# Kernel optimization log

Hardware: AMD Instinct MI355X
Metric: run time of the kernel (lower is better)

Reference implementation:

```python
import jax, jax.numpy as jnp
import numpy as np

EMBED_DIM = 1024
HEADS = 16
D_HEAD = EMBED_DIM // HEADS
B, S = 4, 2048


def setup_inputs() -> dict:
    key = jax.random.key(0)
    ks = jax.random.split(key, 7)
    scale = 1.0 / np.sqrt(EMBED_DIM)
    inp = {
        "key": jax.random.normal(ks[0], (B, S, EMBED_DIM), jnp.float32),
        "query": jax.random.normal(ks[1], (B, S, EMBED_DIM), jnp.float32),
        "value": jax.random.normal(ks[2], (B, S, EMBED_DIM), jnp.float32),
        # causal boolean mask, broadcastable to [B, H, S, S]
        "mask": jnp.tril(jnp.ones((S, S), dtype=bool))[None, None, :, :] * jnp.ones((B, 1, 1, 1), dtype=bool),
        # nn.Linear weights, stored torch-style as [out_features, in_features]
        "Wq": jax.random.normal(ks[3], (EMBED_DIM, EMBED_DIM), jnp.float32) * scale,
        "Wk": jax.random.normal(ks[4], (EMBED_DIM, EMBED_DIM), jnp.float32) * scale,
        "Wv": jax.random.normal(ks[5], (EMBED_DIM, EMBED_DIM), jnp.float32) * scale,
        "Wo": jax.random.normal(ks[6], (EMBED_DIM, EMBED_DIM), jnp.float32) * scale,
    }
    return inp


def reference(key, query, value, mask, Wq, Wk, Wv, Wo):
    # projections (nn.Linear, bias=False): x @ W.T
    q = query @ Wq.T                                    # [B,S,E]
    k = key @ Wk.T
    v = value @ Wv.T
    # split heads -> [B,H,S,d]
    def split(x):
        return x.reshape(B, S, HEADS, D_HEAD).transpose(0, 2, 1, 3)
    q, k, v = split(q), split(k), split(v)
    # scaled dot-product scores [B,H,S,S]
    scores = jnp.einsum("bhqd,bhkd->bhqk", q, k) / np.sqrt(D_HEAD).astype(np.float32)
    scores = jnp.where(mask, scores, jnp.float32(-1e9))
    attn = jax.nn.softmax(scores, axis=-1)
    # attention output, merge heads
    out = jnp.einsum("bhqk,bhkd->bhqd", attn, v)        # [B,H,S,d]
    out = out.transpose(0, 2, 1, 3).reshape(B, S, EMBED_DIM)
    return out @ Wo.T
```

## Files before the change

kernel.cpp:

```cpp
#include <hip/hip_runtime.h>

#define SEQ 2048
#define EMBED 1024
#define DHEAD 64

typedef _Float16 h8 __attribute__((ext_vector_type(8)));
typedef _Float16 h4 __attribute__((ext_vector_type(4)));
typedef float f4 __attribute__((ext_vector_type(4)));
typedef unsigned int u32;

__device__ __forceinline__ void gload_lds16(const void* g, void* l) {
    __builtin_amdgcn_global_load_lds(
        (const __attribute__((address_space(1))) u32*)g,
        (__attribute__((address_space(3))) u32*)l, 16, 0, 0);
}

__global__ __launch_bounds__(256) void cvt_f16(
    const float* __restrict__ q, const float* __restrict__ k, const float* __restrict__ v,
    const float* __restrict__ wq, const float* __restrict__ wk, const float* __restrict__ wv,
    const float* __restrict__ wo,
    _Float16* __restrict__ q16, _Float16* __restrict__ k16, _Float16* __restrict__ v16,
    _Float16* __restrict__ wq16, _Float16* __restrict__ wk16, _Float16* __restrict__ wv16,
    _Float16* __restrict__ wo16)
{
    int bid = blockIdx.x;
    const float* src;
    _Float16* dst;
    float scale = 1.0f;
    size_t base;
    if (bid < 24576) {
        int seg = bid >> 13;
        base = (size_t)(bid & 8191) * 1024 + threadIdx.x * 4;
        src = seg == 0 ? q : seg == 1 ? k : v;
        dst = seg == 0 ? q16 : seg == 1 ? k16 : v16;
    } else {
        int wb = bid - 24576;
        int seg = wb >> 10;
        base = (size_t)(wb & 1023) * 1024 + threadIdx.x * 4;
        src = seg == 0 ? wq : seg == 1 ? wk : seg == 2 ? wv : wo;
        dst = seg == 0 ? wq16 : seg == 1 ? wk16 : seg == 2 ? wv16 : wo16;
        if (seg == 0) scale = 0.18033688011112042f;
    }
    float4 x = *(const float4*)(src + base);
    h4 y = { (_Float16)(x.x * scale), (_Float16)(x.y * scale),
             (_Float16)(x.z * scale), (_Float16)(x.w * scale) };
    *(h4*)(dst + base) = y;
}

__device__ __forceinline__ void gemm_core(const _Float16* __restrict__ A, const _Float16* __restrict__ W,
                                          int m0, int n0, int tid,
                                          _Float16* As, _Float16* Bs, f4 acc[4][4])
{
    const int lane = tid & 63, wave = tid >> 6;
    const int t16 = lane & 15, quad = lane >> 4;
    const int wm = (wave >> 1) * 64, wn = (wave & 1) * 64;
    const int wb = wave * 64;
    const int u0 = tid, u1 = tid + 256;
    const int r0 = u0 >> 2, c0 = u0 & 3;
    const int r1 = u1 >> 2, c1 = u1 & 3;
    const _Float16* ga0 = A + (size_t)(m0 + r0) * 1024 + c0 * 8;
    const _Float16* ga1 = A + (size_t)(m0 + r1) * 1024 + c1 * 8;
    const _Float16* gb0 = W + (size_t)(n0 + r0) * 1024 + c0 * 8;
    const _Float16* gb1 = W + (size_t)(n0 + r1) * 1024 + c1 * 8;
    _Float16* la0 = As + wb * 8;
    _Float16* la1 = As + (256 + wb) * 8;
    _Float16* lb0 = Bs + wb * 8;
    _Float16* lb1 = Bs + (256 + wb) * 8;

    for (int k0 = 0; k0 < 1024; k0 += 32) {
        __syncthreads();
        gload_lds16(ga0 + k0, la0);
        gload_lds16(ga1 + k0, la1);
        gload_lds16(gb0 + k0, lb0);
        gload_lds16(gb1 + k0, lb1);
        __syncthreads();
        h8 af[4], bf[4];
#pragma unroll
        for (int i = 0; i < 4; ++i)
            af[i] = *(const h8*)(As + (wm + i * 16 + t16) * 32 + quad * 8);
#pragma unroll
        for (int j = 0; j < 4; ++j)
            bf[j] = *(const h8*)(Bs + (wn + j * 16 + t16) * 32 + quad * 8);
#pragma unroll
        for (int i = 0; i < 4; ++i)
#pragma unroll
            for (int j = 0; j < 4; ++j)
                acc[i][j] = __builtin_amdgcn_mfma_f32_16x16x32_f16(af[i], bf[j], acc[i][j], 0, 0, 0);
    }
}

__global__ __launch_bounds__(256) void proj_qkv(
    const _Float16* __restrict__ q16, const _Float16* __restrict__ k16, const _Float16* __restrict__ v16,
    const _Float16* __restrict__ Wq, const _Float16* __restrict__ Wk, const _Float16* __restrict__ Wv,
    _Float16* __restrict__ Qh, _Float16* __restrict__ Kh, _Float16* __restrict__ Vt)
{
    __shared__ _Float16 As[4096], Bs[4096];
    const int tid = threadIdx.x;
    const int z = blockIdx.z;
    const _Float16 *A, *W;
    int m0, n0;
    if (z == 2) { A = Wv; W = v16; m0 = blockIdx.y * 128; n0 = blockIdx.x * 128; }
    else if (z == 0) { A = q16; W = Wq; m0 = blockIdx.x * 128; n0 = blockIdx.y * 128; }
    else { A = k16; W = Wk; m0 = blockIdx.x * 128; n0 = blockIdx.y * 128; }

    f4 acc[4][4];
    const f4 z4 = {0.f, 0.f, 0.f, 0.f};
#pragma unroll
    for (int i = 0; i < 4; ++i)
#pragma unroll
        for (int j = 0; j < 4; ++j) acc[i][j] = z4;

    gemm_core(A, W, m0, n0, tid, As, Bs, acc);

    const int lane = tid & 63, wave = tid >> 6;
    const int t16 = lane & 15, quad = lane >> 4;
    const int wm = (wave >> 1) * 64, wn = (wave & 1) * 64;
#pragma unroll
    for (int i = 0; i < 4; ++i)
#pragma unroll
        for (int j = 0; j < 4; ++j)
#pragma unroll
            for (int reg = 0; reg < 4; ++reg) {
                int gm = m0 + wm + i * 16 + quad * 4 + reg;
                int gn = n0 + wn + j * 16 + t16;
                float vv = acc[i][j][reg];
                if (z < 2) {
                    int b = gm >> 11, s = gm & 2047, h = gn >> 6, dd = gn & 63;
                    _Float16* dst = (z == 0) ? Qh : Kh;
                    dst[(((size_t)(b * 16 + h) * SEQ) + s) * DHEAD + dd] = (_Float16)vv;
                } else {
                    int h = gm >> 6, dd = gm & 63, b = gn >> 11, s = gn & 2047;
                    Vt[(((size_t)(b * 16 + h) * DHEAD) + dd) * SEQ + s] = (_Float16)vv;
                }
            }
}

__global__ __launch_bounds__(256) void attn3(
    const _Float16* __restrict__ Qh, const _Float16* __restrict__ Kh,
    const _Float16* __restrict__ Vt, _Float16* __restrict__ Ob)
{
    __shared__ _Float16 Kbuf[2][8][512];
    __shared__ _Float16 Vbuf[2][8][512];
    __shared__ _Float16 Pex[4][2][2][512];

    const int tid = threadIdx.x;
    const int lane = tid & 63, wave = tid >> 6;
    const int t16 = lane & 15, quad = lane >> 4;
    const int bh = blockIdx.x;
    const int b = bh >> 4, h = bh & 15;
    const int qb = (gridDim.y - 1) - blockIdx.y;
    const int q0 = qb * 128;
    const int nqt = qb * 2 + 2;

    const _Float16* Qp = Qh + (size_t)bh * SEQ * DHEAD;
    const _Float16* Kp = Kh + (size_t)bh * SEQ * DHEAD;
    const _Float16* Vp = Vt + (size_t)bh * DHEAD * SEQ;

    const int qlo[2] = { q0 + wave * 32, q0 + wave * 32 + 16 };
    const int last0 = (qlo[0] + 15) >> 6;
    const int last1 = (qlo[1] + 15) >> 6;

    h8 qf[2][2];
#pragma unroll
    for (int qb2 = 0; qb2 < 2; ++qb2)
#pragma unroll
        for (int kc = 0; kc < 2; ++kc)
            qf[qb2][kc] = *(const h8*)(Qp + (size_t)(qlo[qb2] + t16) * 64 + kc * 32 + quad * 8);

    const _Float16* Kl = Kp + t16 * 64 + quad * 8;
    const _Float16* Vl = Vp + t16 * 2048 + quad * 8;

#define STAGE(jt_, bufi)                                                                  \
    do {                                                                                  \
        if (wave < 2) {                                                                   \
            _Pragma("unroll")                                                             \
            for (int i_ = 0; i_ < 4; ++i_) {                                              \
                int g_ = wave * 4 + i_;                                                   \
                gload_lds16(Kl + (jt_) * 4096 + (g_ >> 1) * 1024 + (g_ & 1) * 32,         \
                            &Kbuf[bufi][g_][0]);                                          \
            }                                                                             \
        } else {                                                                          \
            _Pragma("unroll")                                                             \
            for (int i_ = 0; i_ < 4; ++i_) {                                              \
                int g_ = (wave - 2) * 4 + i_;                                             \
                gload_lds16(Vl + (g_ >> 1) * 32768 + (jt_) * 64 + (g_ & 1) * 32,          \
                            &Vbuf[bufi][g_][0]);                                          \
            }                                                                             \
        }                                                                                 \
    } while (0)

    STAGE(0, 0);
    __syncthreads();

    float mv[2] = {-1e30f, -1e30f};
    float lv[2] = {0.f, 0.f};
    f4 o_acc[2][4];
    const f4 z4 = {0.f, 0.f, 0.f, 0.f};
#pragma unroll
    for (int qb2 = 0; qb2 < 2; ++qb2)
#pragma unroll
        for (int dt = 0; dt < 4; ++dt) o_acc[qb2][dt] = z4;

    for (int jt = 0; jt < nqt; ++jt) {
        const int buf = jt & 1;
        if (jt + 1 < nqt) STAGE(jt + 1, buf ^ 1);

        if (jt <= last1) {
            f4 s0[4], s1[4];
#pragma unroll
            for (int j4 = 0; j4 < 4; ++j4) {
                h8 kfa = *(const h8*)(&Kbuf[buf][j4 * 2 + 0][lane * 8]);
                h8 kfb = *(const h8*)(&Kbuf[buf][j4 * 2 + 1][lane * 8]);
                s1[j4] = __builtin_amdgcn_mfma_f32_16x16x32_f16(kfa, qf[1][0], z4, 0, 0, 0);
                s1[j4] = __builtin_amdgcn_mfma_f32_16x16x32_f16(kfb, qf[1][1], s1[j4], 0, 0, 0);
                s0[j4] = __builtin_amdgcn_mfma_f32_16x16x32_f16(kfa, qf[0][0], z4, 0, 0, 0);
                s0[j4] = __builtin_amdgcn_mfma_f32_16x16x32_f16(kfb, qf[0][1], s0[j4], 0, 0, 0);
            }

            auto softmax_store = [&](f4* s, int qb2) {
                const int myq = qlo[qb2] + t16;
                if ((jt << 6) + 63 > myq - t16 + 15 || true) {  }
                if ((jt << 6) + 63 > qlo[qb2]) {
#pragma unroll
                    for (int j4 = 0; j4 < 4; ++j4)
#pragma unroll
                        for (int reg = 0; reg < 4; ++reg) {
                            int kk = (jt << 6) + j4 * 16 + quad * 4 + reg;
                            if (kk > myq) s[j4][reg] = -1e30f;
                        }
                }
                float mr = s[0][0];
#pragma unroll
                for (int j4 = 0; j4 < 4; ++j4)
#pragma unroll
                    for (int reg = 0; reg < 4; ++reg) mr = fmaxf(mr, s[j4][reg]);
                mr = fmaxf(mr, __shfl_xor(mr, 16, 64));
                mr = fmaxf(mr, __shfl_xor(mr, 32, 64));
                float mn = fmaxf(mv[qb2], mr);
                float al = __builtin_amdgcn_exp2f(mv[qb2] - mn);
                mv[qb2] = mn;
                float rs = 0.f;
#pragma unroll
                for (int j4 = 0; j4 < 4; ++j4)
#pragma unroll
                    for (int reg = 0; reg < 4; ++reg) {
                        float p = __builtin_amdgcn_exp2f(s[j4][reg] - mn);
                        s[j4][reg] = p;
                        rs += p;
                    }
                rs += __shfl_xor(rs, 16, 64);
                rs += __shfl_xor(rs, 32, 64);
                lv[qb2] = lv[qb2] * al + rs;
#pragma unroll
                for (int dt = 0; dt < 4; ++dt)
#pragma unroll
                    for (int reg = 0; reg < 4; ++reg) o_acc[qb2][dt][reg] *= al;
#pragma unroll
                for (int j4 = 0; j4 < 4; ++j4) {
                    int Lt = (((j4 & 1) * 2 + (quad >> 1)) << 4) + t16;
                    h4 ph = { (_Float16)s[j4][0], (_Float16)s[j4][1],
                              (_Float16)s[j4][2], (_Float16)s[j4][3] };
                    *(h4*)(&Pex[wave][qb2][j4 >> 1][Lt * 8 + (quad & 1) * 4]) = ph;
                }
            };

            if (jt <= last0) {
                softmax_store(s0, 0);
                softmax_store(s1, 1);
                h8 pb0a = *(const h8*)(&Pex[wave][0][0][lane * 8]);
                h8 pb0b = *(const h8*)(&Pex[wave][0][1][lane * 8]);
                h8 pb1a = *(const h8*)(&Pex[wave][1][0][lane * 8]);
                h8 pb1b = *(const h8*)(&Pex[wave][1][1][lane * 8]);
#pragma unroll
                for (int dt = 0; dt < 4; ++dt) {
                    h8 ava = *(const h8*)(&Vbuf[buf][dt * 2 + 0][lane * 8]);
                    h8 avb = *(const h8*)(&Vbuf[buf][dt * 2 + 1][lane * 8]);
                    o_acc[0][dt] = __builtin_amdgcn_mfma_f32_16x16x32_f16(ava, pb0a, o_acc[0][dt], 0, 0, 0);
                    o_acc[0][dt] = __builtin_amdgcn_mfma_f32_16x16x32_f16(avb, pb0b, o_acc[0][dt], 0, 0, 0);
                    o_acc[1][dt] = __builtin_amdgcn_mfma_f32_16x16x32_f16(ava, pb1a, o_acc[1][dt], 0, 0, 0);
                    o_acc[1][dt] = __builtin_amdgcn_mfma_f32_16x16x32_f16(avb, pb1b, o_acc[1][dt], 0, 0, 0);
                }
            } else {
                softmax_store(s1, 1);
                h8 pb1a = *(const h8*)(&Pex[wave][1][0][lane * 8]);
                h8 pb1b = *(const h8*)(&Pex[wave][1][1][lane * 8]);
#pragma unroll
                for (int dt = 0; dt < 4; ++dt) {
                    h8 ava = *(const h8*)(&Vbuf[buf][dt * 2 + 0][lane * 8]);
                    h8 avb = *(const h8*)(&Vbuf[buf][dt * 2 + 1][lane * 8]);
                    o_acc[1][dt] = __builtin_amdgcn_mfma_f32_16x16x32_f16(ava, pb1a, o_acc[1][dt], 0, 0, 0);
                    o_acc[1][dt] = __builtin_amdgcn_mfma_f32_16x16x32_f16(avb, pb1b, o_acc[1][dt], 0, 0, 0);
                }
            }
        }
        __syncthreads();
    }

#pragma unroll
    for (int qb2 = 0; qb2 < 2; ++qb2) {
        float inv = __builtin_amdgcn_rcpf(lv[qb2]);
        _Float16* ep = &Pex[wave][qb2][0][0];
#pragma unroll
        for (int dt = 0; dt < 4; ++dt) {
            h4 ov = { (_Float16)(o_acc[qb2][dt][0] * inv), (_Float16)(o_acc[qb2][dt][1] * inv),
                      (_Float16)(o_acc[qb2][dt][2] * inv), (_Float16)(o_acc[qb2][dt][3] * inv) };
            *(h4*)(ep + t16 * 64 + dt * 16 + quad * 4) = ov;
        }
        h8 r0 = *(const h8*)(ep + t16 * 64 + quad * 8);
        h8 r1 = *(const h8*)(ep + t16 * 64 + 32 + quad * 8);
        int s = qlo[qb2] + t16;
        _Float16* og = Ob + ((size_t)(b * SEQ + s)) * EMBED + h * DHEAD;
        *(h8*)(og + quad * 8) = r0;
        *(h8*)(og + 32 + quad * 8) = r1;
    }
#undef STAGE
}

__global__ __launch_bounds__(256) void proj_out(
    const _Float16* __restrict__ A, const _Float16* __restrict__ Wo, float* __restrict__ out)
{
    __shared__ _Float16 As[4096], Bs[4096];
    const int tid = threadIdx.x;
    const int m0 = blockIdx.x * 128, n0 = blockIdx.y * 128;
    f4 acc[4][4];
    const f4 z4 = {0.f, 0.f, 0.f, 0.f};
#pragma unroll
    for (int i = 0; i < 4; ++i)
#pragma unroll
        for (int j = 0; j < 4; ++j) acc[i][j] = z4;

    gemm_core(A, Wo, m0, n0, tid, As, Bs, acc);

    const int lane = tid & 63, wave = tid >> 6;
    const int t16 = lane & 15, quad = lane >> 4;
    const int wm = (wave >> 1) * 64, wn = (wave & 1) * 64;
#pragma unroll
    for (int i = 0; i < 4; ++i)
#pragma unroll
        for (int j = 0; j < 4; ++j)
#pragma unroll
            for (int reg = 0; reg < 4; ++reg) {
                int gm = m0 + wm + i * 16 + quad * 4 + reg;
                int gn = n0 + wn + j * 16 + t16;
                out[(size_t)gm * EMBED + gn] = acc[i][j][reg];
            }
}

extern "C" void kernel_launch(void* const* d_in, const int* in_sizes, int n_in,
                              void* d_out, int out_size, void* d_ws, size_t ws_size,
                              hipStream_t stream) {
    const float* key   = (const float*)d_in[0];
    const float* query = (const float*)d_in[1];
    const float* value = (const float*)d_in[2];
    const float* Wq = (const float*)d_in[4];
    const float* Wk = (const float*)d_in[5];
    const float* Wv = (const float*)d_in[6];
    const float* Wo = (const float*)d_in[7];

    char* ws = (char*)d_ws;
    _Float16* v16  = (_Float16*)(ws);
    _Float16* Wq16 = (_Float16*)(ws + (16u << 20));
    _Float16* Wk16 = (_Float16*)(ws + (18u << 20));
    _Float16* Wv16 = (_Float16*)(ws + (20u << 20));
    _Float16* Wo16 = (_Float16*)(ws + (22u << 20));
    _Float16* Qh   = (_Float16*)(ws + (24u << 20));
    _Float16* Kh   = (_Float16*)(ws + (40u << 20));
    _Float16* Vt   = (_Float16*)(ws + (56u << 20));
    _Float16* Ob   = v16;
    _Float16* q16 = (_Float16*)d_out;
    _Float16* k16 = (_Float16*)d_out + 8388608;

    dim3 blk(256);
    cvt_f16<<<dim3(28672), blk, 0, stream>>>(query, key, value, Wq, Wk, Wv, Wo,
                                             q16, k16, v16, Wq16, Wk16, Wv16, Wo16);
    proj_qkv<<<dim3(64, 8, 3), blk, 0, stream>>>(q16, k16, v16, Wq16, Wk16, Wv16, Qh, Kh, Vt);
    attn3<<<dim3(64, 16), blk, 0, stream>>>(Qh, Kh, Vt, Ob);
    proj_out<<<dim3(64, 8), blk, 0, stream>>>(Ob, Wo16, (float*)d_out);
}
```

Baseline: 336.8 us.

## Lazily rescale online softmax, halve P exchange buffer, hoist V loads

```diff
diff --git a/kernel.cpp b/kernel.cpp
--- a/kernel.cpp
+++ b/kernel.cpp
@@ -135,13 +135,13 @@
             }
 }
 
-__global__ __launch_bounds__(256) void attn3(
+__global__ __launch_bounds__(256, 4) void attn3(
     const _Float16* __restrict__ Qh, const _Float16* __restrict__ Kh,
     const _Float16* __restrict__ Vt, _Float16* __restrict__ Ob)
 {
     __shared__ _Float16 Kbuf[2][8][512];
     __shared__ _Float16 Vbuf[2][8][512];
-    __shared__ _Float16 Pex[4][2][2][512];
+    __shared__ _Float16 Pex[4][2][512];
 
     const int tid = threadIdx.x;
     const int lane = tid & 63, wave = tid >> 6;
@@ -158,7 +158,6 @@
 
     const int qlo[2] = { q0 + wave * 32, q0 + wave * 32 + 16 };
     const int last0 = (qlo[0] + 15) >> 6;
-    const int last1 = (qlo[1] + 15) >> 6;
 
     h8 qf[2][2];
 #pragma unroll
@@ -205,7 +204,7 @@
         const int buf = jt & 1;
         if (jt + 1 < nqt) STAGE(jt + 1, buf ^ 1);
 
-        if (jt <= last1) {
+        if (jt <= last0) {
             f4 s0[4], s1[4];
 #pragma unroll
             for (int j4 = 0; j4 < 4; ++j4) {
@@ -216,10 +215,15 @@
                 s0[j4] = __builtin_amdgcn_mfma_f32_16x16x32_f16(kfa, qf[0][0], z4, 0, 0, 0);
                 s0[j4] = __builtin_amdgcn_mfma_f32_16x16x32_f16(kfb, qf[0][1], s0[j4], 0, 0, 0);
             }
+            h8 av[4][2];
+#pragma unroll
+            for (int dt = 0; dt < 4; ++dt) {
+                av[dt][0] = *(const h8*)(&Vbuf[buf][dt * 2 + 0][lane * 8]);
+                av[dt][1] = *(const h8*)(&Vbuf[buf][dt * 2 + 1][lane * 8]);
+            }
 
             auto softmax_store = [&](f4* s, int qb2) {
                 const int myq = qlo[qb2] + t16;
-                if ((jt << 6) + 63 > myq - t16 + 15 || true) {  }
                 if ((jt << 6) + 63 > qlo[qb2]) {
 #pragma unroll
                     for (int j4 = 0; j4 < 4; ++j4)
@@ -236,60 +240,54 @@
                     for (int reg = 0; reg < 4; ++reg) mr = fmaxf(mr, s[j4][reg]);
                 mr = fmaxf(mr, __shfl_xor(mr, 16, 64));
                 mr = fmaxf(mr, __shfl_xor(mr, 32, 64));
-                float mn = fmaxf(mv[qb2], mr);
-                float al = __builtin_amdgcn_exp2f(mv[qb2] - mn);
-                mv[qb2] = mn;
+                float mn = mv[qb2];
+                if (__any(mr > mn + 8.0f)) {
+                    mn = fmaxf(mn, mr);
+                    float al = __builtin_amdgcn_exp2f(mv[qb2] - mn);
+                    mv[qb2] = mn;
+                    lv[qb2] *= al;
+#pragma unroll
+                    for (int dt = 0; dt < 4; ++dt)
+#pragma unroll
+                        for (int reg = 0; reg < 4; ++reg) o_acc[qb2][dt][reg] *= al;
+                }
                 float rs = 0.f;
 #pragma unroll
-                for (int j4 = 0; j4 < 4; ++j4)
+                for (int j4 = 0; j4 < 4; ++j4) {
 #pragma unroll
                     for (int reg = 0; reg < 4; ++reg) {
                         float p = __builtin_amdgcn_exp2f(s[j4][reg] - mn);
                         s[j4][reg] = p;
                         rs += p;
                     }
-                rs += __shfl_xor(rs, 16, 64);
-                rs += __shfl_xor(rs, 32, 64);
-                lv[qb2] = lv[qb2] * al + rs;
-#pragma unroll
-                for (int dt = 0; dt < 4; ++dt)
-#pragma unroll
-                    for (int reg = 0; reg < 4; ++reg) o_acc[qb2][dt][reg] *= al;
-#pragma unroll
-                for (int j4 = 0; j4 < 4; ++j4) {
                     int Lt = (((j4 & 1) * 2 + (quad >> 1)) << 4) + t16;
                     h4 ph = { (_Float16)s[j4][0], (_Float16)s[j4][1],
                               (_Float16)s[j4][2], (_Float16)s[j4][3] };
-                    *(h4*)(&Pex[wave][qb2][j4 >> 1][Lt * 8 + (quad & 1) * 4]) = ph;
-                }
+                    *(h4*)(&Pex[wave][j4 >> 1][Lt * 8 + (quad & 1) * 4]) = ph;
+                }
+                rs += __shfl_xor(rs, 16, 64);
+                rs += __shfl_xor(rs, 32, 64);
+                lv[qb2] += rs;
             };
 
-            if (jt <= last0) {
-                softmax_store(s0, 0);
-                softmax_store(s1, 1);
-                h8 pb0a = *(const h8*)(&Pex[wave][0][0][lane * 8]);
-                h8 pb0b = *(const h8*)(&Pex[wave][0][1][lane * 8]);
-                h8 pb1a = *(const h8*)(&Pex[wave][1][0][lane * 8]);
-                h8 pb1b = *(const h8*)(&Pex[wave][1][1][lane * 8]);
+            softmax_store(s0, 0);
+            {
+                h8 pa = *(const h8*)(&Pex[wave][0][lane * 8]);
+                h8 pb = *(const h8*)(&Pex[wave][1][lane * 8]);
 #pragma unroll
                 for (int dt = 0; dt < 4; ++dt) {
-                    h8 ava = *(const h8*)(&Vbuf[buf][dt * 2 + 0][lane * 8]);
-                    h8 avb = *(const h8*)(&Vbuf[buf][dt * 2 + 1][lane * 8]);
-                    o_acc[0][dt] = __builtin_amdgcn_mfma_f32_16x16x32_f16(ava, pb0a, o_acc[0][dt], 0, 0, 0);
-                    o_acc[0][dt] = __builtin_amdgcn_mfma_f32_16x16x32_f16(avb, pb0b, o_acc[0][dt], 0, 0, 0);
-                    o_acc[1][dt] = __builtin_amdgcn_mfma_f32_16x16x32_f16(ava, pb1a, o_acc[1][dt], 0, 0, 0);
-                    o_acc[1][dt] = __builtin_amdgcn_mfma_f32_16x16x32_f16(avb, pb1b, o_acc[1][dt], 0, 0, 0);
-                }
-            } else {
-                softmax_store(s1, 1);
-                h8 pb1a = *(const h8*)(&Pex[wave][1][0][lane * 8]);
-                h8 pb1b = *(const h8*)(&Pex[wave][1][1][lane * 8]);
+                    o_acc[0][dt] = __builtin_amdgcn_mfma_f32_16x16x32_f16(av[dt][0], pa, o_acc[0][dt], 0, 0, 0);
+                    o_acc[0][dt] = __builtin_amdgcn_mfma_f32_16x16x32_f16(av[dt][1], pb, o_acc[0][dt], 0, 0, 0);
+                }
+            }
+            softmax_store(s1, 1);
+            {
+                h8 pa = *(const h8*)(&Pex[wave][0][lane * 8]);
+                h8 pb = *(const h8*)(&Pex[wave][1][lane * 8]);
 #pragma unroll
                 for (int dt = 0; dt < 4; ++dt) {
-                    h8 ava = *(const h8*)(&Vbuf[buf][dt * 2 + 0][lane * 8]);
-                    h8 avb = *(const h8*)(&Vbuf[buf][dt * 2 + 1][lane * 8]);
-                    o_acc[1][dt] = __builtin_amdgcn_mfma_f32_16x16x32_f16(ava, pb1a, o_acc[1][dt], 0, 0, 0);
-                    o_acc[1][dt] = __builtin_amdgcn_mfma_f32_16x16x32_f16(avb, pb1b, o_acc[1][dt], 0, 0, 0);
+                    o_acc[1][dt] = __builtin_amdgcn_mfma_f32_16x16x32_f16(av[dt][0], pa, o_acc[1][dt], 0, 0, 0);
+                    o_acc[1][dt] = __builtin_amdgcn_mfma_f32_16x16x32_f16(av[dt][1], pb, o_acc[1][dt], 0, 0, 0);
                 }
             }
         }
@@ -299,7 +297,7 @@
 #pragma unroll
     for (int qb2 = 0; qb2 < 2; ++qb2) {
         float inv = __builtin_amdgcn_rcpf(lv[qb2]);
-        _Float16* ep = &Pex[wave][qb2][0][0];
+        _Float16* ep = &Pex[wave][0][0];
 #pragma unroll
         for (int dt = 0; dt < 4; ++dt) {
             h4 ov = { (_Float16)(o_acc[qb2][dt][0] * inv), (_Float16)(o_acc[qb2][dt][1] * inv),
```

Measured after the change: 398.4 us. +18.3%, slower.
